# Optimization experiments

Measured on AMD Instinct MI355X. Metric: run time of the kernel, lower is better.

The kernel has to match this reference:

```python
import jax, jax.numpy as jnp
import numpy as np

LAMBDAS = (1.0, 10.0)
MAX_NEURONS = 12
RECONFIG = 50
INIT_BATCH = 4000
BATCH_INC = 2166
NS = 2  # switch point: normal equations -> QR -> incremental QR


def setup_inputs() -> dict:
    key = jax.random.key(0)
    kx, ky = jax.random.split(key)
    X = jax.random.normal(kx, (30000, 784), dtype=jnp.float32)
    labels = jax.random.randint(ky, (30000,), 0, 10)
    Y = jax.nn.one_hot(labels, 10, dtype=jnp.float32)  # [N, 10] one-hot targets
    return {"X": X, "Y": Y}


def _forward(X, Y, key):
    N, d = X.shape
    n_cand = len(LAMBDAS) * RECONFIG
    lam = jnp.repeat(jnp.asarray(LAMBDAS, dtype=X.dtype), RECONFIG)  # [n_cand]
    H = jnp.zeros((N, MAX_NEURONS), dtype=X.dtype)
    W = jnp.zeros((d, 0), dtype=X.dtype)
    b = jnp.zeros((0,), dtype=X.dtype)
    Q = R = QT = beta = None
    y = Y
    batch_size = INIT_BATCH
    for k in range(MAX_NEURONS):
        key, kperm, kw, kb = jax.random.split(key, 4)
        indices = jax.random.permutation(kperm, N)[:batch_size]
        Xk = X[indices]              # [B, d]
        Tk = Y[indices]              # [B, 10]
        ek = Tk if k == 0 else Tk - y[indices]  # residual on the batch
        # candidate random features, scaled per-lambda
        W_random = lam * (2.0 * jax.random.uniform(kw, (d, n_cand), dtype=X.dtype) - 1.0)
        b_random = lam * (2.0 * jax.random.uniform(kb, (1, n_cand), dtype=X.dtype) - 1.0)
        h = jax.nn.sigmoid(Xk @ W_random + b_random)             # [B, n_cand]
        v = (ek.T @ h) ** 2 / jnp.sum(h * h, axis=0)             # [10, n_cand]
        best = jnp.argmax(jnp.mean(v, axis=0))
        W_c = jax.lax.dynamic_slice_in_dim(W_random, best, 1, axis=1)  # [d, 1]
        b_c = jax.lax.dynamic_slice_in_dim(b_random, best, 1, axis=1)[0]  # [1]
        h_c = jax.nn.sigmoid(X @ W_c + b_c)[:, 0]                # [N]
        H = H.at[:, k].set(h_c)
        W = jnp.concatenate([W, W_c], axis=1)
        b = jnp.concatenate([b, b_c], axis=0)
        Hk = H[:, : k + 1]
        if k < NS:
            beta = jnp.linalg.inv(Hk.T @ Hk) @ (Hk.T @ Y)
        elif k == NS:
            Q, R = jnp.linalg.qr(Hk)
            QT = Q.T @ Y
            beta = jax.scipy.linalg.solve_triangular(R, QT, lower=False)
        else:
            # incremental Gram-Schmidt QR update with the new column h_c
            r1 = Q.T @ h_c                       # [k]
            t = h_c - Q @ r1
            r2 = jnp.linalg.norm(t)
            q = t / r2
            Q = jnp.concatenate([Q, q[:, None]], axis=1)
            R = jnp.block([[R, r1[:, None]],
                           [jnp.zeros((1, k), R.dtype), r2[None, None]]])
            QT = jnp.concatenate([QT, (q @ Y)[None, :]], axis=0)
            beta = jax.scipy.linalg.solve_triangular(R, QT, lower=False)
        y = Hk @ beta
        batch_size += BATCH_INC
    return W, b, beta


def reference(X, Y):
    return _forward(X, Y, jax.random.key(42))
```

## Files before the change

kernel.cpp:

```cpp
#include <hip/hip_runtime.h>
#include <cstdint>
#include <cstddef>
#include <cmath>

#define N_ROWS 30000
#define D_IN   784
#define NC     100
#define NCP    128
#define NSEG   12
#define SEG    30000
#define SORT_BLOCKS 118
#define KP     800
#define MAXBLK 435
#define SL     16

typedef short bf16x8 __attribute__((ext_vector_type(8)));
typedef float f32x4  __attribute__((ext_vector_type(4)));

struct Hdr {
  uint32_t kperm[12][2];
  uint32_t kw[12][2];
  uint32_t kb[12][2];
  uint32_t sub[12][2][2];
  int best; int pad0;
  float bsel;
  float r2, inv_r2;
  float r1s[12 * SL];
  float r1bs[12 * SL];
  float R[144];
  float QT[120];
  float beta[120];
  float den[100];
  float num[1000];
};

__device__ __forceinline__ void tf2x32(uint32_t k0, uint32_t k1,
                                       uint32_t x0, uint32_t x1,
                                       uint32_t& o0, uint32_t& o1) {
  const uint32_t kx = k0 ^ k1 ^ 0x1BD11BDAu;
  x0 += k0; x1 += k1;
  x0 += x1; x1 = (x1<<13)|(x1>>19); x1 ^= x0;
  x0 += x1; x1 = (x1<<15)|(x1>>17); x1 ^= x0;
  x0 += x1; x1 = (x1<<26)|(x1>>6);  x1 ^= x0;
  x0 += x1; x1 = (x1<<6) |(x1>>26); x1 ^= x0;
  x0 += k1; x1 += kx + 1u;
  x0 += x1; x1 = (x1<<17)|(x1>>15); x1 ^= x0;
  x0 += x1; x1 = (x1<<29)|(x1>>3);  x1 ^= x0;
  x0 += x1; x1 = (x1<<16)|(x1>>16); x1 ^= x0;
  x0 += x1; x1 = (x1<<24)|(x1>>8);  x1 ^= x0;
  x0 += kx; x1 += k0 + 2u;
  x0 += x1; x1 = (x1<<13)|(x1>>19); x1 ^= x0;
  x0 += x1; x1 = (x1<<15)|(x1>>17); x1 ^= x0;
  x0 += x1; x1 = (x1<<26)|(x1>>6);  x1 ^= x0;
  x0 += x1; x1 = (x1<<6) |(x1>>26); x1 ^= x0;
  x0 += k0; x1 += k1 + 3u;
  x0 += x1; x1 = (x1<<17)|(x1>>15); x1 ^= x0;
  x0 += x1; x1 = (x1<<29)|(x1>>3);  x1 ^= x0;
  x0 += x1; x1 = (x1<<16)|(x1>>16); x1 ^= x0;
  x0 += x1; x1 = (x1<<24)|(x1>>8);  x1 ^= x0;
  x0 += k1; x1 += kx + 4u;
  x0 += x1; x1 = (x1<<13)|(x1>>19); x1 ^= x0;
  x0 += x1; x1 = (x1<<15)|(x1>>17); x1 ^= x0;
  x0 += x1; x1 = (x1<<26)|(x1>>6);  x1 ^= x0;
  x0 += x1; x1 = (x1<<6) |(x1>>26); x1 ^= x0;
  x0 += kx; x1 += k0 + 5u;
  o0 = x0; o1 = x1;
}

__device__ __forceinline__ float u01(uint32_t bits) {
  return __uint_as_float((bits >> 9) | 0x3f800000u) - 1.0f;
}

__device__ __forceinline__ uint32_t rbits32(uint32_t k0, uint32_t k1, uint32_t idx) {
  uint32_t o0, o1;
  tf2x32(k0, k1, 0u, idx, o0, o1);
  return o0 ^ o1;
}

__device__ __forceinline__ ushort f2bf_rne(float f) {
  uint32_t u = __float_as_uint(f);
  return (ushort)((u + 0x7fffu + ((u >> 16) & 1u)) >> 16);
}
__device__ __forceinline__ float bf2f(ushort h) {
  return __uint_as_float(((uint32_t)h) << 16);
}

__global__ void k_rng_chain(Hdr* h) {
  if (threadIdx.x != 0 || blockIdx.x != 0) return;
  uint32_t c0 = 0u, c1 = 42u;
  for (int k = 0; k < 12; k++) {
    uint32_t t0, t1;
    tf2x32(c0, c1, 0u, 1u, t0, t1); h->kperm[k][0] = t0; h->kperm[k][1] = t1;
    tf2x32(c0, c1, 0u, 2u, t0, t1); h->kw[k][0]   = t0; h->kw[k][1]   = t1;
    tf2x32(c0, c1, 0u, 3u, t0, t1); h->kb[k][0]   = t0; h->kb[k][1]   = t1;
    uint32_t p0 = h->kperm[k][0], p1 = h->kperm[k][1];
    for (int r = 0; r < 2; r++) {
      uint32_t s0, s1, n0, n1;
      tf2x32(p0, p1, 0u, 1u, s0, s1);
      tf2x32(p0, p1, 0u, 0u, n0, n1);
      h->sub[k][r][0] = s0; h->sub[k][r][1] = s1;
      p0 = n0; p1 = n1;
    }
    tf2x32(c0, c1, 0u, 0u, t0, t1); c0 = t0; c1 = t1;
  }
}

__global__ __launch_bounds__(256) void k_sortkeys(const Hdr* __restrict__ h,
    uint32_t* __restrict__ keys, int* __restrict__ vals, int round) {
  int p = blockIdx.x * 256 + threadIdx.x;
  if (p >= NSEG * SEG) return;
  int s = p / SEG, i = p % SEG;
  keys[p] = rbits32(h->sub[s][round][0], h->sub[s][round][1], (uint32_t)i);
  if (round == 0) vals[p] = i;
}

__global__ __launch_bounds__(256) void k_hist(const uint32_t* __restrict__ keys,
    uint32_t* __restrict__ hs, int shift) {
  __shared__ uint32_t hloc[256];
  int s = blockIdx.x / SORT_BLOCKS, b = blockIdx.x % SORT_BLOCKS;
  hloc[threadIdx.x] = 0;
  __syncthreads();
  int i = b * 256 + threadIdx.x;
  if (i < SEG) {
    uint32_t d = (keys[s * SEG + i] >> shift) & 255u;
    atomicAdd(&hloc[d], 1u);
  }
  __syncthreads();
  hs[(size_t)(s * SORT_BLOCKS + b) * 256 + threadIdx.x] = hloc[threadIdx.x];
}

__global__ __launch_bounds__(256) void k_scan(uint32_t* hs) {
  __shared__ uint32_t tot[256];
  __shared__ uint32_t base[256];
  int s = blockIdx.x, d = threadIdx.x;
  uint32_t run = 0;
  for (int b = 0; b < SORT_BLOCKS; b++) {
    size_t idx = (size_t)(s * SORT_BLOCKS + b) * 256 + d;
    uint32_t c = hs[idx];
    hs[idx] = run;
    run += c;
  }
  tot[d] = run;
  __syncthreads();
  if (d == 0) {
    uint32_t acc = 0;
    for (int q = 0; q < 256; q++) { base[q] = acc; acc += tot[q]; }
  }
  __syncthreads();
  uint32_t bb = base[d];
  for (int b = 0; b < SORT_BLOCKS; b++)
    hs[(size_t)(s * SORT_BLOCKS + b) * 256 + d] += bb;
}

__global__ __launch_bounds__(256) void k_scatter(const uint32_t* __restrict__ ik,
    const int* __restrict__ iv, uint32_t* __restrict__ ok, int* __restrict__ ov,
    const uint32_t* __restrict__ hs, int shift) {
  __shared__ uint16_t wh[4][256];
  int s = blockIdx.x / SORT_BLOCKS, b = blockIdx.x % SORT_BLOCKS;
  int tid = threadIdx.x;
  for (int q = tid; q < 1024; q += 256) ((uint16_t*)wh)[q] = 0;
  __syncthreads();
  int i = b * 256 + tid;
  bool valid = (i < SEG);
  uint32_t key = 0, dg = 0; int val = 0;
  if (valid) {
    key = ik[s * SEG + i];
    val = iv[s * SEG + i];
    dg = (key >> shift) & 255u;
  }
  unsigned long long vm = __ballot(valid ? 1 : 0);
  unsigned long long m = ~0ULL;
  for (int bit = 0; bit < 8; bit++) {
    unsigned long long bm = __ballot((int)((dg >> bit) & 1u));
    m &= ((dg >> bit) & 1u) ? bm : ~bm;
  }
  m &= vm;
  int wv = tid >> 6, lane = tid & 63;
  int rw = __popcll(m & ((1ULL << lane) - 1ULL));
  if (valid && rw == 0) wh[wv][dg] = (uint16_t)__popcll(m);
  __syncthreads();
  if (valid) {
    int rank = rw;
    for (int q = 0; q < wv; q++) rank += wh[q][dg];
    uint32_t pos = hs[(size_t)(s * SORT_BLOCKS + b) * 256 + dg] + rank;
    ok[s * SEG + pos] = key;
    ov[s * SEG + pos] = val;
  }
}

__global__ __launch_bounds__(256) void k_gen(const Hdr* __restrict__ h,
    float* __restrict__ Wr, short* __restrict__ Wthi, short* __restrict__ Wtlo) {
  int t = blockIdx.x * 256 + threadIdx.x;
  if (t >= NSEG * NCP * KP) return;
  int seg = t / (NCP * KP);
  int r = t % (NCP * KP);
  int c = r / KP, d = r % KP;
  float val = 0.f;
  if (c < NC && d < D_IN) {
    int n = d * NC + c;
    float u = u01(rbits32(h->kw[seg][0], h->kw[seg][1], (uint32_t)n));
    float lam = (c < 50) ? 1.f : 10.f;
    val = lam * (2.f * u - 1.f);
  }
  ushort hi = f2bf_rne(val);
  ushort lo = f2bf_rne(val - bf2f(hi));
  Wthi[t] = (short)hi;
  Wtlo[t] = (short)lo;
  if (d < D_IN) Wr[(size_t)seg * D_IN * NCP + (size_t)d * NCP + c] = val;
}

__global__ __launch_bounds__(256) void k_genb(const Hdr* __restrict__ h, float* __restrict__ br) {
  int t = blockIdx.x * 256 + threadIdx.x;
  if (t >= NSEG * NC) return;
  int k = t / NC, c = t % NC;
  float u = u01(rbits32(h->kb[k][0], h->kb[k][1], (uint32_t)c));
  float lam = (c < 50) ? 1.f : 10.f;
  br[t] = lam * (2.f * u - 1.f);
}

__global__ __launch_bounds__(256) void k_batch_mfma(const float* __restrict__ X,
    const short* __restrict__ Wthi, const short* __restrict__ Wtlo,
    const float* __restrict__ br, const int* __restrict__ perm,
    const float* __restrict__ Y, const float* __restrict__ yv,
    float* __restrict__ P, int kk, int bs) {
  __shared__ short Ah[64][40], Al[64][40];
  __shared__ short Bh[128][40], Bl[128][40];
  __shared__ int idxs[64];
  __shared__ float ekS[64][10];
  int tid = threadIdx.x;
  int row0 = blockIdx.x * 64;
  if (tid < 64) {
    int rr = row0 + tid;
    idxs[tid] = perm[rr < bs ? rr : (bs - 1)];
  }
  __syncthreads();
  for (int q = tid; q < 640; q += 256) {
    int r = q / 10, j = q % 10;
    float e = 0.f;
    if (row0 + r < bs) {
      int idx = idxs[r];
      e = Y[(size_t)idx * 10 + j];
      if (kk > 0) e -= yv[(size_t)idx * 10 + j];
    }
    ekS[r][j] = e;
  }
  int wave = tid >> 6, lane = tid & 63;
  int kg = lane >> 4, ln = lane & 15;

  f32x4 acc[4][2];
  #pragma unroll
  for (int m = 0; m < 4; m++)
    #pragma unroll
    for (int j = 0; j < 2; j++)
      acc[m][j] = (f32x4){0.f, 0.f, 0.f, 0.f};

  int arow = tid >> 2, aq = tid & 3;
  int bcol = tid >> 1, bh2 = tid & 1;

  for (int k0 = 0; k0 < KP; k0 += 32) {
    __syncthreads();
    {
      int kbase = k0 + aq * 8;
      const float* xr = X + (size_t)idxs[arow] * D_IN;
      float v[8];
      if (kbase + 8 <= D_IN) {
        float4 p0 = *(const float4*)(xr + kbase);
        float4 p1 = *(const float4*)(xr + kbase + 4);
        v[0]=p0.x; v[1]=p0.y; v[2]=p0.z; v[3]=p0.w;
        v[4]=p1.x; v[5]=p1.y; v[6]=p1.z; v[7]=p1.w;
      } else {
        #pragma unroll
        for (int q = 0; q < 8; q++) v[q] = (kbase + q < D_IN) ? xr[kbase + q] : 0.f;
      }
      uint32_t ph[4], pl[4];
      #pragma unroll
      for (int q = 0; q < 4; q++) {
        ushort h0 = f2bf_rne(v[2*q]),   h1 = f2bf_rne(v[2*q+1]);
        ushort l0 = f2bf_rne(v[2*q]   - bf2f(h0));
        ushort l1 = f2bf_rne(v[2*q+1] - bf2f(h1));
        ph[q] = (uint32_t)h0 | ((uint32_t)h1 << 16);
        pl[q] = (uint32_t)l0 | ((uint32_t)l1 << 16);
      }
      *(uint4*)&Ah[arow][aq*8] = make_uint4(ph[0], ph[1], ph[2], ph[3]);
      *(uint4*)&Al[arow][aq*8] = make_uint4(pl[0], pl[1], pl[2], pl[3]);
    }
    {
      int boff = bh2 * 16;
      const uint4* sh = (const uint4*)(Wthi + (size_t)bcol * KP + k0 + boff);
      const uint4* sl = (const uint4*)(Wtlo + (size_t)bcol * KP + k0 + boff);
      uint4 h0 = sh[0], h1 = sh[1], l0 = sl[0], l1 = sl[1];
      *(uint4*)&Bh[bcol][boff]     = h0;
      *(uint4*)&Bh[bcol][boff + 8] = h1;
      *(uint4*)&Bl[bcol][boff]     = l0;
      *(uint4*)&Bl[bcol][boff + 8] = l1;
    }
    __syncthreads();
    bf16x8 bhf[2], blf[2];
    #pragma unroll
    for (int j = 0; j < 2; j++) {
      int n = (2 * wave + j) * 16 + ln;
      bhf[j] = *(bf16x8*)&Bh[n][kg * 8];
      blf[j] = *(bf16x8*)&Bl[n][kg * 8];
    }
    #pragma unroll
    for (int m = 0; m < 4; m++) {
      bf16x8 ah = *(bf16x8*)&Ah[m * 16 + ln][kg * 8];
      bf16x8 al = *(bf16x8*)&Al[m * 16 + ln][kg * 8];
      #pragma unroll
      for (int j = 0; j < 2; j++) {
        acc[m][j] = __builtin_amdgcn_mfma_f32_16x16x32_bf16(ah, bhf[j], acc[m][j], 0, 0, 0);
        acc[m][j] = __builtin_amdgcn_mfma_f32_16x16x32_bf16(ah, blf[j], acc[m][j], 0, 0, 0);
        acc[m][j] = __builtin_amdgcn_mfma_f32_16x16x32_bf16(al, bhf[j], acc[m][j], 0, 0, 0);
      }
    }
  }
  #pragma unroll
  for (int j = 0; j < 2; j++) {
    int col = (2 * wave + j) * 16 + ln;
    float bias = (col < NC) ? br[col] : 0.f;
    float den_t = 0.f;
    float num_t[10];
    #pragma unroll
    for (int q = 0; q < 10; q++) num_t[q] = 0.f;
    #pragma unroll
    for (int m = 0; m < 4; m++) {
      #pragma unroll
      for (int r = 0; r < 4; r++) {
        int rl = m * 16 + kg * 4 + r;
        if (row0 + rl < bs) {
          float hsig = 1.f / (1.f + expf(-(acc[m][j][r] + bias)));
          den_t += hsig * hsig;
          #pragma unroll
          for (int q = 0; q < 10; q++) num_t[q] += hsig * ekS[rl][q];
        }
      }
    }
    den_t += __shfl_xor(den_t, 16, 64);
    den_t += __shfl_xor(den_t, 32, 64);
    #pragma unroll
    for (int q = 0; q < 10; q++) {
      num_t[q] += __shfl_xor(num_t[q], 16, 64);
      num_t[q] += __shfl_xor(num_t[q], 32, 64);
    }
    if (kg == 0 && col < NC) {
      float* dst = P + (size_t)blockIdx.x * 1100 + col * 11;
      dst[0] = den_t;
      #pragma unroll
      for (int q = 0; q < 10; q++) dst[1 + q] = num_t[q];
    }
  }
}

__global__ __launch_bounds__(256) void k_score(const float* __restrict__ P, Hdr* h, int nblk) {
  int c = blockIdx.x;
  int tid = threadIdx.x;
  int q = tid % 11, g = tid / 11;
  float acc = 0.f;
  if (tid < 253) {
    for (int b = g; b < nblk; b += 23)
      acc += P[(size_t)b * 1100 + c * 11 + q];
  }
  __shared__ float red[23][11];
  if (tid < 253) red[g][q] = acc;
  __syncthreads();
  if (tid < 11) {
    float s = 0.f;
    #pragma unroll
    for (int g2 = 0; g2 < 23; g2++) s += red[g2][tid];
    if (tid == 0) h->den[c] = s;
    else h->num[c * 10 + tid - 1] = s;
  }
}

__global__ __launch_bounds__(256) void k_select(Hdr* h, const float* __restrict__ brk,
    const float* __restrict__ Wr, float* __restrict__ wcol,
    float* __restrict__ outW, float* __restrict__ outB, int k) {
  __shared__ int sbest;
  int tid = threadIdx.x;
  if (tid < 12 * SL) { h->r1s[tid] = 0.f; h->r1bs[tid] = 0.f; }
  if (tid == 0) {
    float best = -1.f; int bi = 0;
    for (int c = 0; c < NC; c++) {
      float s = 0.f;
      for (int j = 0; j < 10; j++) { float n = h->num[c * 10 + j]; s += n * n; }
      float v = s / (h->den[c] * 10.f);
      if (v > best) { best = v; bi = c; }
    }
    h->best = bi;
    h->bsel = brk[bi];
    outB[k] = h->bsel;
    sbest = bi;
  }
  __syncthreads();
  int best = sbest;
  for (int d = tid; d < D_IN; d += 256) {
    float v = Wr[(size_t)d * NCP + best];
    wcol[d] = v;
    outW[d * 12 + k] = v;
  }
}

__global__ __launch_bounds__(256) void k_hc(const float* __restrict__ X,
    const Hdr* __restrict__ h, const float* __restrict__ wcol,
    float* __restrict__ H, float* __restrict__ hc, int k) {
  int lane = threadIdx.x & 63;
  int row = blockIdx.x * 4 + (threadIdx.x >> 6);
  if (row >= N_ROWS) return;
  const float4* xp = (const float4*)(X + (size_t)row * D_IN);
  const float4* wp = (const float4*)wcol;
  float acc = 0.f;
  #pragma unroll
  for (int it = 0; it < 4; it++) {
    int p = lane + it * 64;
    if (p < 196) {
      float4 xv = xp[p], wv = wp[p];
      acc += xv.x * wv.x + xv.y * wv.y + xv.z * wv.z + xv.w * wv.w;
    }
  }
  #pragma unroll
  for (int o = 32; o > 0; o >>= 1) acc += __shfl_xor(acc, o, 64);
  if (lane == 0) {
    float hv = 1.f / (1.f + expf(-(acc + h->bsel)));
    H[(size_t)row * 12 + k] = hv;
    hc[row] = hv;
  }
}

__global__ __launch_bounds__(256) void k_dotQ(const float* __restrict__ Qcm,
    const float* __restrict__ vec, float* __restrict__ dst) {
  int j = blockIdx.x / SL, sl = blockIdx.x % SL;
  const float* q = Qcm + (size_t)j * N_ROWS;
  int i0 = sl * (N_ROWS / SL);
  int i1 = i0 + (N_ROWS / SL);
  float a = 0.f;
  for (int i = i0 + threadIdx.x; i < i1; i += 256) a += q[i] * vec[i];
  __shared__ float red[256];
  red[threadIdx.x] = a;
  __syncthreads();
  for (int s = 128; s > 0; s >>= 1) {
    if (threadIdx.x < s) red[threadIdx.x] += red[threadIdx.x + s];
    __syncthreads();
  }
  if (threadIdx.x == 0) dst[j * SL + sl] = red[0];
}

__global__ __launch_bounds__(256) void k_sub(float* __restrict__ Qcm,
    const float* __restrict__ basev, const float* __restrict__ coefp,
    const float* __restrict__ Y, float* __restrict__ partials, int k) {
  __shared__ float cf[12];
  int tid = threadIdx.x;
  if (tid < 12) {
    float s = 0.f;
    #pragma unroll
    for (int s8 = 0; s8 < SL; s8++) s += coefp[tid * SL + s8];
    cf[tid] = s;
  }
  __syncthreads();
  int i = blockIdx.x * 256 + tid;
  float t = 0.f;
  float v[11];
  #pragma unroll
  for (int q = 0; q < 11; q++) v[q] = 0.f;
  if (i < N_ROWS) {
    t = basev[i];
    for (int j = 0; j < k; j++) t -= Qcm[(size_t)j * N_ROWS + i] * cf[j];
    Qcm[(size_t)k * N_ROWS + i] = t;
    const float* yr = Y + (size_t)i * 10;
    #pragma unroll
    for (int q = 0; q < 10; q++) v[q] = t * yr[q];
    v[10] = t * t;
  }
  #pragma unroll
  for (int o = 1; o < 64; o <<= 1) {
    #pragma unroll
    for (int q = 0; q < 11; q++) v[q] += __shfl_xor(v[q], o, 64);
  }
  __shared__ float wred[4][11];
  int wave = tid >> 6, lane = tid & 63;
  if (lane == 0) {
    #pragma unroll
    for (int q = 0; q < 11; q++) wred[wave][q] = v[q];
  }
  __syncthreads();
  if (tid < 11) {
    float s = wred[0][tid] + wred[1][tid] + wred[2][tid] + wred[3][tid];
    partials[blockIdx.x * 12 + tid] = s;
  }
}

__global__ __launch_bounds__(256) void k_fin(Hdr* h, const float* __restrict__ partials,
    float* __restrict__ out_beta, int k) {
  int tid = threadIdx.x;
  __shared__ float red[23][11];
  int q = tid % 11, g = tid / 11;
  float acc = 0.f;
  if (tid < 253) {
    for (int b = g; b < SORT_BLOCKS; b += 23)
      acc += partials[b * 12 + q];
  }
  if (tid < 253) red[g][q] = acc;
  __syncthreads();
  __shared__ float s[11];
  __shared__ float Rcol[12];
  __shared__ float r2s;
  if (tid < 11) {
    float ss = 0.f;
    #pragma unroll
    for (int g2 = 0; g2 < 23; g2++) ss += red[g2][tid];
    s[tid] = ss;
  }
  __syncthreads();
  if (tid == 0) {
    float r2 = sqrtf(s[10]);
    h->r2 = r2;
    h->inv_r2 = 1.f / r2;
    h->R[k * 12 + k] = r2;
    r2s = r2;
    Rcol[k] = r2;
    for (int i = 0; i < k; i++) {
      float rs = 0.f;
      #pragma unroll
      for (int s8 = 0; s8 < SL; s8++) rs += h->r1s[i * SL + s8] + h->r1bs[i * SL + s8];
      h->R[i * 12 + k] = rs;
      Rcol[i] = rs;
    }
  }
  __syncthreads();
  if (tid < 10) {
    float qtk = s[tid] / r2s;
    h->QT[k * 10 + tid] = qtk;
    float bloc[12];
    for (int i = k; i >= 0; i--) {
      float t = (i == k) ? qtk : h->QT[i * 10 + tid];
      for (int m = i + 1; m <= k; m++) {
        float Rim = (m == k) ? Rcol[i] : h->R[i * 12 + m];
        t -= Rim * bloc[m];
      }
      t /= ((i == k) ? r2s : h->R[i * 12 + i]);
      bloc[i] = t;
      h->beta[i * 10 + tid] = t;
      out_beta[i * 10 + tid] = t;
    }
  }
}

__global__ __launch_bounds__(256) void k_y_qnorm(Hdr* h,
    const float* __restrict__ H, float* __restrict__ y, float* __restrict__ Qk, int k) {
  __shared__ float sb[120];
  int tid = threadIdx.x;
  if (tid < 120) sb[tid] = h->beta[tid];
  float ir = h->inv_r2;
  __syncthreads();
  int i = blockIdx.x * 256 + tid;
  if (i < N_ROWS) {
    Qk[i] *= ir;
    float hr[12];
    for (int m = 0; m <= k; m++) hr[m] = H[(size_t)i * 12 + m];
    #pragma unroll
    for (int j = 0; j < 10; j++) {
      float a = 0.f;
      for (int m = 0; m <= k; m++) a += hr[m] * sb[m * 10 + j];
      y[(size_t)i * 10 + j] = a;
    }
  }
}

static inline int cdiv(int a, int b) { return (a + b - 1) / b; }

extern "C" void kernel_launch(void* const* d_in, const int* in_sizes, int n_in,
                              void* d_out, int out_size, void* d_ws, size_t ws_size,
                              hipStream_t stream) {
  const float* X = (const float*)d_in[0];
  const float* Y = (const float*)d_in[1];
  float* out = (float*)d_out;
  float* outW = out;
  float* outB = out + 9408;
  float* outBeta = out + 9420;

  char* base = (char*)d_ws;
  Hdr* hdr = (Hdr*)base;
  float* r1p  = (float*)(base + offsetof(Hdr, r1s));
  float* r1bp = (float*)(base + offsetof(Hdr, r1bs));

  size_t off = 16384;
  auto nxt = [&](size_t bytes) -> void* {
    void* p = base + off;
    off += (bytes + 255) & ~(size_t)255;
    return p;
  };
  uint32_t* keysA = (uint32_t*)nxt((size_t)NSEG * SEG * 4);
  uint32_t* keysB = (uint32_t*)nxt((size_t)NSEG * SEG * 4);
  int* valsA = (int*)nxt((size_t)NSEG * SEG * 4);
  int* valsB = (int*)nxt((size_t)NSEG * SEG * 4);
  uint32_t* hs = (uint32_t*)nxt((size_t)NSEG * SORT_BLOCKS * 256 * 4);
  float* WrAll = (float*)nxt((size_t)NSEG * D_IN * NCP * 4);
  short* WthiAll = (short*)nxt((size_t)NSEG * NCP * KP * 2);
  short* WtloAll = (short*)nxt((size_t)NSEG * NCP * KP * 2);
  float* brAll = (float*)nxt((size_t)NSEG * NC * 4);
  float* wcol = (float*)nxt((size_t)D_IN * 4);
  float* Pbuf = (float*)nxt((size_t)MAXBLK * 1100 * 4);
  float* Qcm = (float*)nxt((size_t)12 * N_ROWS * 4);
  float* Hbuf = (float*)nxt((size_t)N_ROWS * 12 * 4);
  float* hcbuf = (float*)nxt((size_t)N_ROWS * 4);
  float* ybuf = (float*)nxt((size_t)N_ROWS * 10 * 4);
  float* partials = (float*)nxt(128 * 12 * 4);

  k_rng_chain<<<1, 64, 0, stream>>>(hdr);

  const int keygrid = cdiv(NSEG * SEG, 256);
  const int sortgrid = NSEG * SORT_BLOCKS;
  for (int round = 0; round < 2; round++) {
    k_sortkeys<<<keygrid, 256, 0, stream>>>(hdr, keysA, valsA, round);
    for (int pass = 0; pass < 4; pass++) {
      uint32_t* ik = (pass & 1) ? keysB : keysA;
      uint32_t* ok = (pass & 1) ? keysA : keysB;
      int* iv = (pass & 1) ? valsB : valsA;
      int* ov = (pass & 1) ? valsA : valsB;
      k_hist<<<sortgrid, 256, 0, stream>>>(ik, hs, 8 * pass);
      k_scan<<<NSEG, 256, 0, stream>>>(hs);
      k_scatter<<<sortgrid, 256, 0, stream>>>(ik, iv, ok, ov, hs, 8 * pass);
    }
  }

  k_gen<<<cdiv(NSEG * NCP * KP, 256), 256, 0, stream>>>(hdr, WrAll, WthiAll, WtloAll);
  k_genb<<<cdiv(NSEG * NC, 256), 256, 0, stream>>>(hdr, brAll);

  for (int k = 0; k < 12; k++) {
    int bs = 4000 + 2166 * k;
    int nblk = cdiv(bs, 64);
    const int* perm = valsA + (size_t)k * SEG;
    const short* Wthi = WthiAll + (size_t)k * NCP * KP;
    const short* Wtlo = WtloAll + (size_t)k * NCP * KP;
    const float* brk = brAll + (size_t)k * NC;

    k_batch_mfma<<<nblk, 256, 0, stream>>>(X, Wthi, Wtlo, brk, perm, Y, ybuf, Pbuf, k, bs);
    k_score<<<NC, 256, 0, stream>>>(Pbuf, hdr, nblk);
    k_select<<<1, 256, 0, stream>>>(hdr, brk, WrAll + (size_t)k * D_IN * NCP, wcol, outW, outB, k);
    k_hc<<<7500, 256, 0, stream>>>(X, hdr, wcol, Hbuf, hcbuf, k);
    if (k > 0) k_dotQ<<<k * SL, 256, 0, stream>>>(Qcm, hcbuf, r1p);
    k_sub<<<SORT_BLOCKS, 256, 0, stream>>>(Qcm, hcbuf, r1p, Y, partials, k);
    if (k == 1 || k == 2) {
      k_dotQ<<<k * SL, 256, 0, stream>>>(Qcm, Qcm + (size_t)k * N_ROWS, r1bp);
      k_sub<<<SORT_BLOCKS, 256, 0, stream>>>(Qcm, Qcm + (size_t)k * N_ROWS, r1bp, Y, partials, k);
    }
    k_fin<<<1, 256, 0, stream>>>(hdr, partials, outBeta, k);
    k_y_qnorm<<<SORT_BLOCKS, 256, 0, stream>>>(hdr, Hbuf, ybuf, Qcm + (size_t)k * N_ROWS, k);
  }
}
```

Measured before the change: 1.714 ms.

## Fuse score/select and sub/fin via ticket atomics, drop y buffer and qnorm kernel

Merges k_score with k_select and k_sub with k_fin, using a last-block atomic ticket so each pair needs one launch. The residual y is now computed on the fly inside the batch kernel from H and beta, and Q is kept unnormalized with the 1/r2 scaling folded into the coefficients, so k_y_qnorm and the ybuf writes go away. The radix-sort scan buffers its loads and passes the digit base as a separate array instead of rewriting the histogram. This removes several small launches and memory passes per iteration, at the cost of threadfence/atomic synchronization and extra per-row work in the batch kernel.

```diff
diff --git a/kernel.cpp b/kernel.cpp
--- a/kernel.cpp
+++ b/kernel.cpp
@@ -24,7 +24,7 @@
   uint32_t sub[12][2][2];
   int best; int pad0;
   float bsel;
-  float r2, inv_r2;
+  float r2arr[12];
   float r1s[12 * SL];
   float r1bs[12 * SL];
   float R[144];
@@ -129,16 +129,24 @@
   hs[(size_t)(s * SORT_BLOCKS + b) * 256 + threadIdx.x] = hloc[threadIdx.x];
 }
 
-__global__ __launch_bounds__(256) void k_scan(uint32_t* hs) {
+__global__ __launch_bounds__(256) void k_scan(uint32_t* hs, uint32_t* baseA) {
   __shared__ uint32_t tot[256];
   __shared__ uint32_t base[256];
   int s = blockIdx.x, d = threadIdx.x;
   uint32_t run = 0;
-  for (int b = 0; b < SORT_BLOCKS; b++) {
-    size_t idx = (size_t)(s * SORT_BLOCKS + b) * 256 + d;
-    uint32_t c = hs[idx];
-    hs[idx] = run;
-    run += c;
+  uint32_t buf[30];
+  for (int c0 = 0; c0 < SORT_BLOCKS; c0 += 30) {
+    int n = SORT_BLOCKS - c0; if (n > 30) n = 30;
+    #pragma unroll
+    for (int j = 0; j < 30; j++)
+      if (j < n) buf[j] = hs[(size_t)(s * SORT_BLOCKS + c0 + j) * 256 + d];
+    #pragma unroll
+    for (int j = 0; j < 30; j++)
+      if (j < n) {
+        uint32_t c = buf[j];
+        hs[(size_t)(s * SORT_BLOCKS + c0 + j) * 256 + d] = run;
+        run += c;
+      }
   }
   tot[d] = run;
   __syncthreads();
@@ -147,14 +155,12 @@
     for (int q = 0; q < 256; q++) { base[q] = acc; acc += tot[q]; }
   }
   __syncthreads();
-  uint32_t bb = base[d];
-  for (int b = 0; b < SORT_BLOCKS; b++)
-    hs[(size_t)(s * SORT_BLOCKS + b) * 256 + d] += bb;
+  baseA[s * 256 + d] = base[d];
 }
 
 __global__ __launch_bounds__(256) void k_scatter(const uint32_t* __restrict__ ik,
     const int* __restrict__ iv, uint32_t* __restrict__ ok, int* __restrict__ ov,
-    const uint32_t* __restrict__ hs, int shift) {
+    const uint32_t* __restrict__ hs, const uint32_t* __restrict__ baseA, int shift) {
   __shared__ uint16_t wh[4][256];
   int s = blockIdx.x / SORT_BLOCKS, b = blockIdx.x % SORT_BLOCKS;
   int tid = threadIdx.x;
@@ -182,7 +188,7 @@
   if (valid) {
     int rank = rw;
     for (int q = 0; q < wv; q++) rank += wh[q][dg];
-    uint32_t pos = hs[(size_t)(s * SORT_BLOCKS + b) * 256 + dg] + rank;
+    uint32_t pos = hs[(size_t)(s * SORT_BLOCKS + b) * 256 + dg] + baseA[s * 256 + dg] + rank;
     ok[s * SEG + pos] = key;
     ov[s * SEG + pos] = val;
   }
@@ -221,26 +227,39 @@
 __global__ __launch_bounds__(256) void k_batch_mfma(const float* __restrict__ X,
     const short* __restrict__ Wthi, const short* __restrict__ Wtlo,
     const float* __restrict__ br, const int* __restrict__ perm,
-    const float* __restrict__ Y, const float* __restrict__ yv,
-    float* __restrict__ P, int kk, int bs) {
+    const float* __restrict__ Y, const float* __restrict__ Hbuf,
+    const Hdr* __restrict__ hd, float* __restrict__ P, int kk, int bs) {
   __shared__ short Ah[64][40], Al[64][40];
   __shared__ short Bh[128][40], Bl[128][40];
   __shared__ int idxs[64];
   __shared__ float ekS[64][10];
+  __shared__ float hS[64][12];
+  __shared__ float betaS[120];
   int tid = threadIdx.x;
   int row0 = blockIdx.x * 64;
   if (tid < 64) {
     int rr = row0 + tid;
     idxs[tid] = perm[rr < bs ? rr : (bs - 1)];
   }
+  if (kk > 0 && tid < kk * 10) betaS[tid] = hd->beta[tid];
+  __syncthreads();
+  if (kk > 0) {
+    for (int q = tid; q < 64 * kk; q += 256) {
+      int r = q / kk, m = q % kk;
+      hS[r][m] = Hbuf[(size_t)idxs[r] * 12 + m];
+    }
+  }
   __syncthreads();
   for (int q = tid; q < 640; q += 256) {
     int r = q / 10, j = q % 10;
     float e = 0.f;
     if (row0 + r < bs) {
-      int idx = idxs[r];
-      e = Y[(size_t)idx * 10 + j];
-      if (kk > 0) e -= yv[(size_t)idx * 10 + j];
+      e = Y[(size_t)idxs[r] * 10 + j];
+      if (kk > 0) {
+        float yv = 0.f;
+        for (int m = 0; m < kk; m++) yv += hS[r][m] * betaS[m * 10 + j];
+        e -= yv;
+      }
     }
     ekS[r][j] = e;
   }
@@ -351,7 +370,10 @@
   }
 }
 
-__global__ __launch_bounds__(256) void k_score(const float* __restrict__ P, Hdr* h, int nblk) {
+__global__ __launch_bounds__(256) void k_score_select(const float* __restrict__ P,
+    Hdr* h, const float* __restrict__ brk, const float* __restrict__ Wr,
+    float* __restrict__ wcol, float* __restrict__ outW, float* __restrict__ outB,
+    int* __restrict__ ticket, int k, int nblk) {
   int c = blockIdx.x;
   int tid = threadIdx.x;
   int q = tid % 11, g = tid / 11;
@@ -370,21 +392,25 @@
     if (tid == 0) h->den[c] = s;
     else h->num[c * 10 + tid - 1] = s;
   }
-}
-
-__global__ __launch_bounds__(256) void k_select(Hdr* h, const float* __restrict__ brk,
-    const float* __restrict__ Wr, float* __restrict__ wcol,
-    float* __restrict__ outW, float* __restrict__ outB, int k) {
+  __shared__ int sdone;
+  __syncthreads();
+  __threadfence();
+  if (tid == 0) {
+    int old = atomicAdd(ticket, 1);
+    sdone = (old == NC - 1) ? 1 : 0;
+  }
+  __syncthreads();
+  if (!sdone) return;
+  __threadfence();
   __shared__ int sbest;
-  int tid = threadIdx.x;
   if (tid < 12 * SL) { h->r1s[tid] = 0.f; h->r1bs[tid] = 0.f; }
   if (tid == 0) {
     float best = -1.f; int bi = 0;
-    for (int c = 0; c < NC; c++) {
+    for (int cc = 0; cc < NC; cc++) {
       float s = 0.f;
-      for (int j = 0; j < 10; j++) { float n = h->num[c * 10 + j]; s += n * n; }
-      float v = s / (h->den[c] * 10.f);
-      if (v > best) { best = v; bi = c; }
+      for (int j = 0; j < 10; j++) { float n = h->num[cc * 10 + j]; s += n * n; }
+      float v = s / (h->den[cc] * 10.f);
+      if (v > best) { best = v; bi = cc; }
     }
     h->best = bi;
     h->bsel = brk[bi];
@@ -426,10 +452,10 @@
   }
 }
 
-__global__ __launch_bounds__(256) void k_dotQ(const float* __restrict__ Qcm,
+__global__ __launch_bounds__(256) void k_dotQ(const float* __restrict__ Tcm,
     const float* __restrict__ vec, float* __restrict__ dst) {
   int j = blockIdx.x / SL, sl = blockIdx.x % SL;
-  const float* q = Qcm + (size_t)j * N_ROWS;
+  const float* q = Tcm + (size_t)j * N_ROWS;
   int i0 = sl * (N_ROWS / SL);
   int i1 = i0 + (N_ROWS / SL);
   float a = 0.f;
@@ -444,16 +470,18 @@
   if (threadIdx.x == 0) dst[j * SL + sl] = red[0];
 }
 
-__global__ __launch_bounds__(256) void k_sub(float* __restrict__ Qcm,
+__global__ __launch_bounds__(256) void k_sub_fin(Hdr* h, float* __restrict__ Tcm,
     const float* __restrict__ basev, const float* __restrict__ coefp,
-    const float* __restrict__ Y, float* __restrict__ partials, int k) {
+    const float* __restrict__ Y, float* __restrict__ partials,
+    float* __restrict__ out_beta, int* __restrict__ ticket, int k, int dofin) {
   __shared__ float cf[12];
   int tid = threadIdx.x;
   if (tid < 12) {
     float s = 0.f;
     #pragma unroll
     for (int s8 = 0; s8 < SL; s8++) s += coefp[tid * SL + s8];
-    cf[tid] = s;
+    float r2j = (tid < k) ? h->r2arr[tid] : 1.f;
+    cf[tid] = s / (r2j * r2j);
   }
   __syncthreads();
   int i = blockIdx.x * 256 + tid;
@@ -463,13 +491,16 @@
   for (int q = 0; q < 11; q++) v[q] = 0.f;
   if (i < N_ROWS) {
     t = basev[i];
-    for (int j = 0; j < k; j++) t -= Qcm[(size_t)j * N_ROWS + i] * cf[j];
-    Qcm[(size_t)k * N_ROWS + i] = t;
-    const float* yr = Y + (size_t)i * 10;
-    #pragma unroll
-    for (int q = 0; q < 10; q++) v[q] = t * yr[q];
-    v[10] = t * t;
-  }
+    for (int j = 0; j < k; j++) t -= Tcm[(size_t)j * N_ROWS + i] * cf[j];
+    Tcm[(size_t)k * N_ROWS + i] = t;
+    if (dofin) {
+      const float* yr = Y + (size_t)i * 10;
+      #pragma unroll
+      for (int q = 0; q < 10; q++) v[q] = t * yr[q];
+      v[10] = t * t;
+    }
+  }
+  if (!dofin) return;
   #pragma unroll
   for (int o = 1; o < 64; o <<= 1) {
     #pragma unroll
@@ -486,19 +517,24 @@
     float s = wred[0][tid] + wred[1][tid] + wred[2][tid] + wred[3][tid];
     partials[blockIdx.x * 12 + tid] = s;
   }
-}
-
-__global__ __launch_bounds__(256) void k_fin(Hdr* h, const float* __restrict__ partials,
-    float* __restrict__ out_beta, int k) {
-  int tid = threadIdx.x;
+  __shared__ int sdone;
+  __syncthreads();
+  __threadfence();
+  if (tid == 0) {
+    int old = atomicAdd(ticket, 1);
+    sdone = (old == SORT_BLOCKS - 1) ? 1 : 0;
+  }
+  __syncthreads();
+  if (!sdone) return;
+  __threadfence();
   __shared__ float red[23][11];
   int q = tid % 11, g = tid / 11;
-  float acc = 0.f;
+  float acc2 = 0.f;
   if (tid < 253) {
     for (int b = g; b < SORT_BLOCKS; b += 23)
-      acc += partials[b * 12 + q];
-  }
-  if (tid < 253) red[g][q] = acc;
+      acc2 += partials[b * 12 + q];
+  }
+  if (tid < 253) red[g][q] = acc2;
   __syncthreads();
   __shared__ float s[11];
   __shared__ float Rcol[12];
@@ -512,17 +548,17 @@
   __syncthreads();
   if (tid == 0) {
     float r2 = sqrtf(s[10]);
-    h->r2 = r2;
-    h->inv_r2 = 1.f / r2;
+    h->r2arr[k] = r2;
     h->R[k * 12 + k] = r2;
     r2s = r2;
     Rcol[k] = r2;
-    for (int i = 0; i < k; i++) {
+    for (int i2 = 0; i2 < k; i2++) {
       float rs = 0.f;
       #pragma unroll
-      for (int s8 = 0; s8 < SL; s8++) rs += h->r1s[i * SL + s8] + h->r1bs[i * SL + s8];
-      h->R[i * 12 + k] = rs;
-      Rcol[i] = rs;
+      for (int s8 = 0; s8 < SL; s8++) rs += h->r1s[i2 * SL + s8] + h->r1bs[i2 * SL + s8];
+      float Rik = rs / h->r2arr[i2];
+      h->R[i2 * 12 + k] = Rik;
+      Rcol[i2] = Rik;
     }
   }
   __syncthreads();
@@ -530,37 +566,16 @@
     float qtk = s[tid] / r2s;
     h->QT[k * 10 + tid] = qtk;
     float bloc[12];
-    for (int i = k; i >= 0; i--) {
-      float t = (i == k) ? qtk : h->QT[i * 10 + tid];
-      for (int m = i + 1; m <= k; m++) {
-        float Rim = (m == k) ? Rcol[i] : h->R[i * 12 + m];
-        t -= Rim * bloc[m];
+    for (int i2 = k; i2 >= 0; i2--) {
+      float t2 = (i2 == k) ? qtk : h->QT[i2 * 10 + tid];
+      for (int m = i2 + 1; m <= k; m++) {
+        float Rim = (m == k) ? Rcol[i2] : h->R[i2 * 12 + m];
+        t2 -= Rim * bloc[m];
       }
-      t /= ((i == k) ? r2s : h->R[i * 12 + i]);
-      bloc[i] = t;
-      h->beta[i * 10 + tid] = t;
-      out_beta[i * 10 + tid] = t;
-    }
-  }
-}
-
-__global__ __launch_bounds__(256) void k_y_qnorm(Hdr* h,
-    const float* __restrict__ H, float* __restrict__ y, float* __restrict__ Qk, int k) {
-  __shared__ float sb[120];
-  int tid = threadIdx.x;
-  if (tid < 120) sb[tid] = h->beta[tid];
-  float ir = h->inv_r2;
-  __syncthreads();
-  int i = blockIdx.x * 256 + tid;
-  if (i < N_ROWS) {
-    Qk[i] *= ir;
-    float hr[12];
-    for (int m = 0; m <= k; m++) hr[m] = H[(size_t)i * 12 + m];
-    #pragma unroll
-    for (int j = 0; j < 10; j++) {
-      float a = 0.f;
-      for (int m = 0; m <= k; m++) a += hr[m] * sb[m * 10 + j];
-      y[(size_t)i * 10 + j] = a;
+      t2 /= ((i2 == k) ? r2s : h->R[i2 * 12 + i2]);
+      bloc[i2] = t2;
+      h->beta[i2 * 10 + tid] = t2;
+      out_beta[i2 * 10 + tid] = t2;
     }
   }
 }
@@ -588,22 +603,25 @@
     off += (bytes + 255) & ~(size_t)255;
     return p;
   };
+  int* tickets = (int*)nxt(256);
   uint32_t* keysA = (uint32_t*)nxt((size_t)NSEG * SEG * 4);
   uint32_t* keysB = (uint32_t*)nxt((size_t)NSEG * SEG * 4);
   int* valsA = (int*)nxt((size_t)NSEG * SEG * 4);
   int* valsB = (int*)nxt((size_t)NSEG * SEG * 4);
   uint32_t* hs = (uint32_t*)nxt((size_t)NSEG * SORT_BLOCKS * 256 * 4);
+  uint32_t* baseA = (uint32_t*)nxt((size_t)NSEG * 256 * 4);
   float* WrAll = (float*)nxt((size_t)NSEG * D_IN * NCP * 4);
   short* WthiAll = (short*)nxt((size_t)NSEG * NCP * KP * 2);
   short* WtloAll = (short*)nxt((size_t)NSEG * NCP * KP * 2);
   float* brAll = (float*)nxt((size_t)NSEG * NC * 4);
   float* wcol = (float*)nxt((size_t)D_IN * 4);
   float* Pbuf = (float*)nxt((size_t)MAXBLK * 1100 * 4);
-  float* Qcm = (float*)nxt((size_t)12 * N_ROWS * 4);
+  float* Tcm = (float*)nxt((size_t)12 * N_ROWS * 4);
   float* Hbuf = (float*)nxt((size_t)N_ROWS * 12 * 4);
   float* hcbuf = (float*)nxt((size_t)N_ROWS * 4);
-  float* ybuf = (float*)nxt((size_t)N_ROWS * 10 * 4);
   float* partials = (float*)nxt(128 * 12 * 4);
+
+  hipMemsetAsync(tickets, 0, 256, stream);
 
   k_rng_chain<<<1, 64, 0, stream>>>(hdr);
 
@@ -617,8 +635,8 @@
       int* iv = (pass & 1) ? valsB : valsA;
       int* ov = (pass & 1) ? valsA : valsB;
       k_hist<<<sortgrid, 256, 0, stream>>>(ik, hs, 8 * pass);
-      k_scan<<<NSEG, 256, 0, stream>>>(hs);
-      k_scatter<<<sortgrid, 256, 0, stream>>>(ik, iv, ok, ov, hs, 8 * pass);
+      k_scan<<<NSEG, 256, 0, stream>>>(hs, baseA);
+      k_scatter<<<sortgrid, 256, 0, stream>>>(ik, iv, ok, ov, hs, baseA, 8 * pass);
     }
   }
 
@@ -633,17 +651,20 @@
     const short* Wtlo = WtloAll + (size_t)k * NCP * KP;
     const float* brk = brAll + (size_t)k * NC;
 
-    k_batch_mfma<<<nblk, 256, 0, stream>>>(X, Wthi, Wtlo, brk, perm, Y, ybuf, Pbuf, k, bs);
-    k_score<<<NC, 256, 0, stream>>>(Pbuf, hdr, nblk);
-    k_select<<<1, 256, 0, stream>>>(hdr, brk, WrAll + (size_t)k * D_IN * NCP, wcol, outW, outB, k);
+    k_batch_mfma<<<nblk, 256, 0, stream>>>(X, Wthi, Wtlo, brk, perm, Y, Hbuf, hdr, Pbuf, k, bs);
+    k_score_select<<<NC, 256, 0, stream>>>(Pbuf, hdr, brk,
+        WrAll + (size_t)k * D_IN * NCP, wcol, outW, outB, &tickets[k], k, nblk);
     k_hc<<<7500, 256, 0, stream>>>(X, hdr, wcol, Hbuf, hcbuf, k);
-    if (k > 0) k_dotQ<<<k * SL, 256, 0, stream>>>(Qcm, hcbuf, r1p);
-    k_sub<<<SORT_BLOCKS, 256, 0, stream>>>(Qcm, hcbuf, r1p, Y, partials, k);
+    if (k > 0) k_dotQ<<<k * SL, 256, 0, stream>>>(Tcm, hcbuf, r1p);
     if (k == 1 || k == 2) {
-      k_dotQ<<<k * SL, 256, 0, stream>>>(Qcm, Qcm + (size_t)k * N_ROWS, r1bp);
-      k_sub<<<SORT_BLOCKS, 256, 0, stream>>>(Qcm, Qcm + (size_t)k * N_ROWS, r1bp, Y, partials, k);
-    }
-    k_fin<<<1, 256, 0, stream>>>(hdr, partials, outBeta, k);
-    k_y_qnorm<<<SORT_BLOCKS, 256, 0, stream>>>(hdr, Hbuf, ybuf, Qcm + (size_t)k * N_ROWS, k);
-  }
-}
+      k_sub_fin<<<SORT_BLOCKS, 256, 0, stream>>>(hdr, Tcm, hcbuf, r1p, Y, partials,
+          outBeta, &tickets[32 + k], k, 0);
+      k_dotQ<<<k * SL, 256, 0, stream>>>(Tcm, Tcm + (size_t)k * N_ROWS, r1bp);
+      k_sub_fin<<<SORT_BLOCKS, 256, 0, stream>>>(hdr, Tcm, Tcm + (size_t)k * N_ROWS, r1bp,
+          Y, partials, outBeta, &tickets[32 + k], k, 1);
+    } else {
+      k_sub_fin<<<SORT_BLOCKS, 256, 0, stream>>>(hdr, Tcm, hcbuf, r1p, Y, partials,
+          outBeta, &tickets[32 + k], k, 1);
+    }
+  }
+}
```

Result: faster. 1.647 ms (-3.9%).
